# Kernel tuning notes

Measured on AMD Instinct MI355X. Metric: run time of the kernel, lower is better.

## Reference

```python
import jax, jax.numpy as jnp
import numpy as np

NUM_HEADS = 12
HEAD_DIM = 64
EPS = 1e-6


def _layernorm(x, g, b):
    mu = jnp.mean(x, axis=-1, keepdims=True)
    var = jnp.mean(jnp.square(x - mu), axis=-1, keepdims=True)
    return (x - mu) * jax.lax.rsqrt(var + EPS) * g + b


def setup_inputs() -> dict:
    key = jax.random.key(0)
    ks = jax.random.split(key, 8)
    D, DFF = 768, 3072
    s = lambda d: 1.0 / np.sqrt(d)
    return {
        "hidden_states": jax.random.normal(ks[0], (4, 2048, D), jnp.float32),
        "ln1_g": jnp.ones((D,), jnp.float32),
        "ln1_b": jnp.zeros((D,), jnp.float32),
        "w_qkv": jax.random.normal(ks[1], (D, 3 * D), jnp.float32) * s(D),
        "b_qkv": jnp.zeros((3 * D,), jnp.float32),
        "w_attn": jax.random.normal(ks[2], (D, D), jnp.float32) * s(D),
        "b_attn": jnp.zeros((D,), jnp.float32),
        "ln2_g": jnp.ones((D,), jnp.float32),
        "ln2_b": jnp.zeros((D,), jnp.float32),
        "w_in": jax.random.normal(ks[3], (D, DFF), jnp.float32) * s(D),
        "b_in": jnp.zeros((DFF,), jnp.float32),
        "w_out": jax.random.normal(ks[4], (DFF, D), jnp.float32) * s(DFF),
        "b_out": jnp.zeros((D,), jnp.float32),
    }


def reference(hidden_states, ln1_g, ln1_b, w_qkv, b_qkv, w_attn, b_attn,
              ln2_g, ln2_b, w_in, b_in, w_out, b_out):
    B, S, D = hidden_states.shape
    residual = hidden_states
    h = _layernorm(hidden_states, ln1_g, ln1_b)
    # QKV: [B,S,3D] -> [B,S,3,H,hd] -> [3,B,H,S,hd]
    qkv = (h @ w_qkv + b_qkv).reshape(B, S, 3, NUM_HEADS, HEAD_DIM)
    qkv = jnp.transpose(qkv, (2, 0, 3, 1, 4))
    scale = HEAD_DIM ** (-0.5)
    q, k, v = qkv[0] * scale, qkv[1], qkv[2]
    scores = jnp.einsum("bhqd,bhkd->bhqk", q, k)
    attn = jax.nn.softmax(scores, axis=-1)
    o = jnp.einsum("bhqk,bhkd->bhqd", attn, v)
    o = jnp.transpose(o, (0, 2, 1, 3)).reshape(B, S, D)
    h = residual + (o @ w_attn + b_attn)
    residual2 = h
    h2 = _layernorm(h, ln2_g, ln2_b)
    h2 = jax.nn.gelu(h2 @ w_in + b_in, approximate=False)
    h2 = h2 @ w_out + b_out
    return residual2 + h2
```

## Files before the change

### kernel.cpp

```cpp
#include <hip/hip_runtime.h>

typedef __bf16 bf16_t;
typedef bf16_t bf16x8 __attribute__((ext_vector_type(8)));
typedef float f32x4 __attribute__((ext_vector_type(4)));
typedef unsigned short ushortx8 __attribute__((ext_vector_type(8)));
typedef unsigned short ushortx4 __attribute__((ext_vector_type(4)));
typedef short short4v __attribute__((ext_vector_type(4)));

union UB8 { bf16_t h8[8]; bf16x8 b; };

__device__ __forceinline__ unsigned short f2bf(float f) {
  union { bf16_t h; unsigned short u; } cv;
  cv.h = (bf16_t)f;
  return cv.u;
}

__device__ __forceinline__ void gl_lds16(const unsigned short* g, unsigned short* l) {
  __builtin_amdgcn_global_load_lds((const __attribute__((address_space(1))) void*)g,
                                   (__attribute__((address_space(3))) void*)l,
                                   16, 0, 0);
}

__device__ __forceinline__ float gelu_fast(float v) {
  float v3 = v * v * v;
  float z = -2.30211886f * v - 0.102945f * v3;
  float e = exp2f(z);
  return v * __builtin_amdgcn_rcpf(1.0f + e);
}

__global__ __launch_bounds__(256) void ln_kernel(const float* __restrict__ x,
                                                 const float* __restrict__ g,
                                                 const float* __restrict__ b,
                                                 unsigned short* __restrict__ out) {
  int row = blockIdx.x;
  int t = threadIdx.x;
  const float* xr = x + (size_t)row * 768;
  float v0 = xr[t], v1 = xr[t + 256], v2 = xr[t + 512];
  __shared__ float red[4];
  float s = v0 + v1 + v2;
  for (int o = 32; o > 0; o >>= 1) s += __shfl_down(s, o, 64);
  if ((t & 63) == 0) red[t >> 6] = s;
  __syncthreads();
  float mu = (red[0] + red[1] + red[2] + red[3]) * (1.0f / 768.0f);
  __syncthreads();
  float d0 = v0 - mu, d1 = v1 - mu, d2 = v2 - mu;
  s = d0 * d0 + d1 * d1 + d2 * d2;
  for (int o = 32; o > 0; o >>= 1) s += __shfl_down(s, o, 64);
  if ((t & 63) == 0) red[t >> 6] = s;
  __syncthreads();
  float var = (red[0] + red[1] + red[2] + red[3]) * (1.0f / 768.0f);
  float rs = rsqrtf(var + 1e-6f);
  unsigned short* orow = out + (size_t)row * 768;
  orow[t]       = f2bf(d0 * rs * g[t]       + b[t]);
  orow[t + 256] = f2bf(d1 * rs * g[t + 256] + b[t + 256]);
  orow[t + 512] = f2bf(d2 * rs * g[t + 512] + b[t + 512]);
}

__global__ __launch_bounds__(256) void transpose_all(
    const float* __restrict__ w_qkv, const float* __restrict__ w_attn,
    const float* __restrict__ w_in, const float* __restrict__ w_out,
    unsigned short* __restrict__ wqkvT, unsigned short* __restrict__ wattnT,
    unsigned short* __restrict__ winT, unsigned short* __restrict__ woutT) {
  int id = blockIdx.x;
  const float* W; unsigned short* WT; int K, N, nx, ny;
  if (id < 1728)      { W = w_qkv;  WT = wqkvT;  K = 768;  N = 2304; nx = id % 72; ny = id / 72; }
  else if (id < 2304) { id -= 1728; W = w_attn; WT = wattnT; K = 768;  N = 768;  nx = id % 24; ny = id / 24; }
  else if (id < 4608) { id -= 2304; W = w_in;   WT = winT;   K = 768;  N = 3072; nx = id % 96; ny = id / 96; }
  else                { id -= 4608; W = w_out;  WT = woutT;  K = 3072; N = 768;  nx = id % 24; ny = id / 24; }
  __shared__ float tile[32][33];
  int n0 = nx * 32, k0 = ny * 32;
  int tx = threadIdx.x, ty = threadIdx.y;
  for (int i = 0; i < 4; i++)
    tile[ty + i * 8][tx] = W[(size_t)(k0 + ty + i * 8) * N + n0 + tx];
  __syncthreads();
  for (int i = 0; i < 4; i++)
    WT[(size_t)(n0 + ty + i * 8) * K + k0 + tx] = f2bf(tile[tx][ty + i * 8]);
}

template <int EPI>
__device__ __forceinline__ void gemm_body(const unsigned short* __restrict__ A,
                                          const unsigned short* __restrict__ BT,
                                          const float* __restrict__ bias,
                                          const float* resid,
                                          void* out, unsigned short* vt, int os,
                                          int N, int K) {
  constexpr int TM = 128, BK = 32, MI = 4;
  constexpr int ASZ = TM * BK;
  constexpr int BUF = ASZ + 128 * BK;
  __shared__ __align__(16) unsigned short smem[3 * BUF];

  int t = threadIdx.x;
  int w = t >> 6, lane = t & 63, ln = lane & 15, quad = lane >> 4;
  int wm = w & 1, wn = w >> 1;

  int gx = gridDim.x;
  int nwg = gx * gridDim.y;
  int flat = blockIdx.y * gx + blockIdx.x;
  int nf = (flat & 7) * (nwg >> 3) + (flat >> 3);
  int m0 = (nf / gx) * TM, n0 = (nf % gx) * 128;

  int lrow = lane >> 2;
  int lslot = lane & 3;
  int scol = (lslot ^ ((lrow >> 1) & 3)) * 8;

  const unsigned short* gA0 = A + (size_t)(m0 + w * 16 + lrow) * K + scol;
  const unsigned short* gA1 = gA0 + (size_t)64 * K;
  const unsigned short* gB0 = BT + (size_t)(n0 + w * 16 + lrow) * K + scol;
  const unsigned short* gB1 = gB0 + (size_t)64 * K;

  auto stage = [&](int buf) {
    unsigned short* Sb = smem + buf * BUF;
    gl_lds16(gA0, Sb + w * 512);
    gl_lds16(gA1, Sb + 2048 + w * 512);
    gl_lds16(gB0, Sb + ASZ + w * 512);
    gl_lds16(gB1, Sb + ASZ + 2048 + w * 512);
    gA0 += BK; gA1 += BK; gB0 += BK; gB1 += BK;
  };

  f32x4 acc[MI][4];
  f32x4 zero = {0.f, 0.f, 0.f, 0.f};
  for (int mi = 0; mi < MI; mi++)
    for (int ni = 0; ni < 4; ni++) acc[mi][ni] = zero;

  int nk = K / BK;
  stage(0);
  stage(1);
  int cur = 0;
  int soff = (quad ^ ((ln >> 1) & 3)) * 8;
  for (int kt = 0; kt < nk; kt++) {
    if (kt < nk - 1) { asm volatile("s_waitcnt vmcnt(4)" ::: "memory"); }
    else             { asm volatile("s_waitcnt vmcnt(0)" ::: "memory"); }
    __builtin_amdgcn_s_barrier();
    __builtin_amdgcn_sched_barrier(0);
    int pre = cur + 2; if (pre >= 3) pre -= 3;
    if (kt + 2 < nk) stage(pre);
    const unsigned short* Sc = smem + cur * BUF;
    bf16x8 af[MI], bfr[4];
#pragma unroll
    for (int mi = 0; mi < MI; mi++)
      af[mi] = *(const bf16x8*)&Sc[(wm * 64 + mi * 16 + ln) * 32 + soff];
#pragma unroll
    for (int ni = 0; ni < 4; ni++)
      bfr[ni] = *(const bf16x8*)&Sc[ASZ + (wn * 64 + ni * 16 + ln) * 32 + soff];
#pragma unroll
    for (int mi = 0; mi < MI; mi++)
#pragma unroll
      for (int ni = 0; ni < 4; ni++)
        acc[mi][ni] = __builtin_amdgcn_mfma_f32_16x16x32_bf16(af[mi], bfr[ni],
                                                              acc[mi][ni], 0, 0, 0);
    cur = cur + 1; if (cur >= 3) cur = 0;
  }

  if (EPI == 2) {
    float* outp = (float*)out;
    for (int mi = 0; mi < MI; mi++) {
      for (int ni = 0; ni < 4; ni++) {
        int col = n0 + wn * 64 + ni * 16 + ln;
        float bv = bias[col];
        for (int r = 0; r < 4; r++) {
          int row = m0 + wm * 64 + mi * 16 + quad * 4 + r;
          float v = acc[mi][ni][r] + bv;
          v += resid[(size_t)row * N + col];
          outp[(size_t)row * N + col] = v;
        }
      }
    }
  } else {
    __syncthreads();
    unsigned short* Cs16 = smem + w * 1024;
    unsigned short* outp = (unsigned short*)out;
    for (int mi = 0; mi < MI; mi++) {
      for (int ni = 0; ni < 4; ni++) {
        int col = n0 + wn * 64 + ni * 16 + ln;
        float bv = bias[col];
        for (int r = 0; r < 4; r++) {
          float v = acc[mi][ni][r] + bv;
          if (EPI == 0) {
            if (col < 768) v *= 0.18033688f;
          } else {
            v = gelu_fast(v);
          }
          Cs16[(quad * 4 + r) * 64 + ni * 16 + ln] = f2bf(v);
        }
      }
      __syncthreads();
      if (EPI == 0 && n0 >= 1536) {
        int c = n0 - 1536 + wn * 64 + lane;
        int s0 = m0 + wm * 64 + mi * 16;
        int bb = s0 >> 11, sl = s0 & 2047;
        ushortx8 lo, hi;
        for (int r = 0; r < 8; r++) lo[r] = Cs16[r * 64 + lane];
        for (int r = 0; r < 8; r++) hi[r] = Cs16[(8 + r) * 64 + lane];
        size_t vbase = ((size_t)(bb * 768 + c)) * 2048 + sl;
        *(ushortx8*)&vt[vbase] = lo;
        *(ushortx8*)&vt[vbase + 8] = hi;
      } else {
        int OS = (EPI == 0) ? os : N;
        for (int j = 0; j < 2; j++) {
          int rrow = j * 8 + (lane >> 3);
          int ch = (lane & 7) * 8;
          ushortx8 pv = *(const ushortx8*)&Cs16[rrow * 64 + ch];
          *(ushortx8*)&outp[(size_t)(m0 + wm * 64 + mi * 16 + rrow) * OS +
                            n0 + wn * 64 + ch] = pv;
        }
      }
      __syncthreads();
    }
  }
}

__global__ __launch_bounds__(256) void gemm_qkv(const unsigned short* A,
    const unsigned short* BT, const float* bias, void* out, unsigned short* vt,
    int N, int K) {
  gemm_body<0>(A, BT, bias, nullptr, out, vt, 1536, N, K);
}
__global__ __launch_bounds__(256) void gemm_attnout(const unsigned short* A,
    const unsigned short* BT, const float* bias, const float* resid, void* out,
    int N, int K) {
  gemm_body<2>(A, BT, bias, resid, out, nullptr, N, N, K);
}
__global__ __launch_bounds__(256) void gemm_ffn1(const unsigned short* A,
    const unsigned short* BT, const float* bias, void* out, int N, int K) {
  gemm_body<1>(A, BT, bias, nullptr, out, nullptr, N, N, K);
}
__global__ __launch_bounds__(256) void gemm_ffn2(const unsigned short* A,
    const unsigned short* BT, const float* bias, const float* resid, void* out,
    int N, int K) {
  gemm_body<2>(A, BT, bias, resid, out, nullptr, N, N, K);
}

__global__ __launch_bounds__(512, 4) void flash_attn(
    const unsigned short* __restrict__ qk, const unsigned short* __restrict__ v_t,
    unsigned short* __restrict__ o) {
  int flat = blockIdx.y * 16 + blockIdx.x;
  int nf = (flat & 7) * 96 + (flat >> 3);
  int qt = nf % 16;
  int bh = nf / 16;
  int b = bh / 12, h = bh % 12;
  int t = threadIdx.x;
  int w = t >> 6, lane = t & 63, ln = lane & 15, quad = lane >> 4;
  int qg = w & 3, kh2 = w >> 2;

  __shared__ __align__(16) unsigned short smem[18432];
  int qrow0 = b * 2048 + qt * 128;
  int qw = qrow0 + qg * 32;

  bf16x8 qf[2][2];
  for (int qi = 0; qi < 2; qi++)
    for (int kh = 0; kh < 2; kh++)
      qf[qi][kh] = *(const bf16x8*)&qk[(size_t)(qw + qi * 16 + ln) * 1536 +
                                      h * 64 + kh * 32 + quad * 8];

  UB8 ones8;
#pragma unroll
  for (int r = 0; r < 8; r++) ones8.h8[r] = (bf16_t)1.0f;

  f32x4 zero = {0.f, 0.f, 0.f, 0.f};
  f32x4 o_acc[4][2];
  for (int df = 0; df < 4; df++)
    for (int qi = 0; qi < 2; qi++) o_acc[df][qi] = zero;
  f32x4 l_acc[2] = {zero, zero};

  int sr = t >> 3, sc = (t & 7) * 8;
  int ssr = (sr & 32) | (((sr >> 2) & 1) << 4) | (((sr >> 3) & 3) << 2) | (sr & 3);
  ushortx8 kreg = *(const ushortx8*)&qk[(size_t)(b * 2048 + sr) * 1536 + 768 + h * 64 + sc];
  ushortx8 vreg = *(const ushortx8*)&v_t[(size_t)(bh * 64 + sr) * 2048 + sc];

  for (int kt = 0; kt < 32; kt++) {
    unsigned short* Ks = smem + (kt & 1) * 9216;
    unsigned short* Vt = Ks + 4608;
    *(ushortx8*)&Ks[ssr * 72 + sc] = kreg;
    *(ushortx8*)&Vt[sr * 72 + sc] = vreg;
    __syncthreads();
    if (kt < 31) {
      int krow0 = b * 2048 + (kt + 1) * 64;
      kreg = *(const ushortx8*)&qk[(size_t)(krow0 + sr) * 1536 + 768 + h * 64 + sc];
      vreg = *(const ushortx8*)&v_t[(size_t)(bh * 64 + sr) * 2048 + (kt + 1) * 64 + sc];
    }

    UB8 pb[2];
#pragma unroll
    for (int kf = 0; kf < 2; kf++) {
      int krow = kh2 * 32 + kf * 16;
      f32x4 ST[2] = {zero, zero};
      bf16x8 kA0 = *(const bf16x8*)&Ks[(krow + ln) * 72 + quad * 8];
      bf16x8 kA1 = *(const bf16x8*)&Ks[(krow + ln) * 72 + 32 + quad * 8];
      __builtin_amdgcn_s_setprio(1);
#pragma unroll
      for (int qi = 0; qi < 2; qi++) {
        ST[qi] = __builtin_amdgcn_mfma_f32_16x16x32_bf16(kA0, qf[qi][0], ST[qi], 0, 0, 0);
        ST[qi] = __builtin_amdgcn_mfma_f32_16x16x32_bf16(kA1, qf[qi][1], ST[qi], 0, 0, 0);
      }
      __builtin_amdgcn_s_setprio(0);
#pragma unroll
      for (int qi = 0; qi < 2; qi++)
#pragma unroll
        for (int r = 0; r < 4; r++)
          pb[qi].h8[kf * 4 + r] = (bf16_t)__builtin_amdgcn_exp2f(ST[qi][r]);
    }
    __builtin_amdgcn_s_setprio(1);
#pragma unroll
    for (int qi = 0; qi < 2; qi++)
      l_acc[qi] = __builtin_amdgcn_mfma_f32_16x16x32_bf16(ones8.b, pb[qi].b,
                                                          l_acc[qi], 0, 0, 0);
#pragma unroll
    for (int df = 0; df < 4; df++) {
      bf16x8 vA = *(const bf16x8*)&Vt[(df * 16 + ln) * 72 + kh2 * 32 + quad * 8];
#pragma unroll
      for (int qi = 0; qi < 2; qi++)
        o_acc[df][qi] = __builtin_amdgcn_mfma_f32_16x16x32_bf16(vA, pb[qi].b,
                                                                o_acc[df][qi], 0, 0, 0);
    }
    __builtin_amdgcn_s_setprio(0);
  }

  __syncthreads();
  float* fb = (float*)smem;
  float* fbl = fb + 8320;
  if (kh2 == 1) {
    for (int df = 0; df < 4; df++)
      for (int qi = 0; qi < 2; qi++)
        for (int r = 0; r < 4; r++)
          fb[qg * 2080 + (qi * 16 + ln) * 65 + df * 16 + quad * 4 + r] =
              o_acc[df][qi][r];
    if (quad == 0)
      for (int qi = 0; qi < 2; qi++)
        fbl[qg * 32 + qi * 16 + ln] = l_acc[qi][0];
  }
  __syncthreads();
  float inv[2];
  if (kh2 == 0) {
    for (int qi = 0; qi < 2; qi++) {
      float lt = l_acc[qi][0] + fbl[qg * 32 + qi * 16 + ln];
      inv[qi] = __builtin_amdgcn_rcpf(lt);
    }
    for (int df = 0; df < 4; df++)
      for (int qi = 0; qi < 2; qi++)
        for (int r = 0; r < 4; r++)
          o_acc[df][qi][r] += fb[qg * 2080 + (qi * 16 + ln) * 65 + df * 16 + quad * 4 + r];
  }
  __syncthreads();
  if (kh2 == 0) {
    unsigned short* Osm = smem + qg * 2304;
    for (int qi = 0; qi < 2; qi++)
      for (int df = 0; df < 4; df++)
        for (int r = 0; r < 4; r++)
          Osm[(qi * 16 + ln) * 72 + df * 16 + quad * 4 + r] =
              f2bf(o_acc[df][qi][r] * inv[qi]);
  }
  __syncthreads();
  if (kh2 == 0) {
    unsigned short* Osm = smem + qg * 2304;
    for (int p2 = 0; p2 < 4; p2++) {
      int rr = p2 * 8 + (lane >> 3);
      int ch = (lane & 7) * 8;
      ushortx8 u = *(const ushortx8*)&Osm[rr * 72 + ch];
      *(ushortx8*)&o[(size_t)(qw + rr) * 768 + h * 64 + ch] = u;
    }
  }
}

extern "C" void kernel_launch(void* const* d_in, const int* in_sizes, int n_in,
                              void* d_out, int out_size, void* d_ws, size_t ws_size,
                              hipStream_t stream) {
  const float* hidden = (const float*)d_in[0];
  const float* ln1_g  = (const float*)d_in[1];
  const float* ln1_b  = (const float*)d_in[2];
  const float* w_qkv  = (const float*)d_in[3];
  const float* b_qkv  = (const float*)d_in[4];
  const float* w_attn = (const float*)d_in[5];
  const float* b_attn = (const float*)d_in[6];
  const float* ln2_g  = (const float*)d_in[7];
  const float* ln2_b  = (const float*)d_in[8];
  const float* w_in   = (const float*)d_in[9];
  const float* b_in   = (const float*)d_in[10];
  const float* w_out  = (const float*)d_in[11];
  const float* b_out  = (const float*)d_in[12];
  float* out = (float*)d_out;

  char* ws = (char*)d_ws;
  unsigned short* wqkvT  = (unsigned short*)(ws + 0);
  unsigned short* wattnT = (unsigned short*)(ws + 3538944);
  unsigned short* winT   = (unsigned short*)(ws + 4718592);
  unsigned short* woutT  = (unsigned short*)(ws + 9437184);
  unsigned short* bufX   = (unsigned short*)(ws + 14155776);
  unsigned short* bufBig = (unsigned short*)(ws + 26738688);
  unsigned short* bufQK  = bufBig;
  unsigned short* v_t    = (unsigned short*)(ws + 26738688 + 25165824);

  transpose_all<<<6912, dim3(32, 8), 0, stream>>>(w_qkv, w_attn, w_in, w_out,
                                                  wqkvT, wattnT, winT, woutT);
  ln_kernel<<<8192, 256, 0, stream>>>(hidden, ln1_g, ln1_b, bufX);
  gemm_qkv<<<dim3(18, 64), 256, 0, stream>>>(bufX, wqkvT, b_qkv, (void*)bufQK,
                                             v_t, 2304, 768);
  flash_attn<<<dim3(16, 48), 512, 0, stream>>>(bufQK, v_t, bufX);
  gemm_attnout<<<dim3(6, 64), 256, 0, stream>>>(bufX, wattnT, b_attn, hidden,
                                                (void*)out, 768, 768);
  ln_kernel<<<8192, 256, 0, stream>>>(out, ln2_g, ln2_b, bufX);
  gemm_ffn1<<<dim3(24, 64), 256, 0, stream>>>(bufX, winT, b_in, (void*)bufBig,
                                              3072, 768);
  gemm_ffn2<<<dim3(6, 64), 256, 0, stream>>>(bufBig, woutT, b_out, out,
                                             (void*)out, 768, 3072);
}
```

Baseline: 382.3 us.

## Split-K FFN2 with atomic accumulation and use 64-row tiles for attn-out GEMM

The attention output projection now uses a 64-row M tile, doubling its grid to 768 blocks so more compute units are occupied. The FFN2 GEMM is split across two K chunks along grid z, and each chunk atomically adds its partial result into the output, which already holds the residual. Only the first chunk adds the bias. This raises parallelism for the skinny N=768 GEMMs, at the cost of fp32 atomic traffic and summation order that is no longer deterministic.

```diff
diff --git a/kernel.cpp b/kernel.cpp
--- a/kernel.cpp
+++ b/kernel.cpp
@@ -77,14 +77,14 @@
     WT[(size_t)(n0 + ty + i * 8) * K + k0 + tx] = f2bf(tile[tx][ty + i * 8]);
 }
 
-template <int EPI>
+template <int EPI, int TM>
 __device__ __forceinline__ void gemm_body(const unsigned short* __restrict__ A,
                                           const unsigned short* __restrict__ BT,
                                           const float* __restrict__ bias,
                                           const float* resid,
                                           void* out, unsigned short* vt, int os,
                                           int N, int K) {
-  constexpr int TM = 128, BK = 32, MI = 4;
+  constexpr int BK = 32, MI = TM / 32;
   constexpr int ASZ = TM * BK;
   constexpr int BUF = ASZ + 128 * BK;
   __shared__ __align__(16) unsigned short smem[3 * BUF];
@@ -99,22 +99,25 @@
   int nf = (flat & 7) * (nwg >> 3) + (flat >> 3);
   int m0 = (nf / gx) * TM, n0 = (nf % gx) * 128;
 
+  int Kc = (EPI == 3) ? (K / (int)gridDim.z) : K;
+  int kbase = (EPI == 3) ? ((int)blockIdx.z * Kc) : 0;
+
   int lrow = lane >> 2;
   int lslot = lane & 3;
   int scol = (lslot ^ ((lrow >> 1) & 3)) * 8;
 
-  const unsigned short* gA0 = A + (size_t)(m0 + w * 16 + lrow) * K + scol;
+  const unsigned short* gA0 = A + (size_t)(m0 + w * 16 + lrow) * K + kbase + scol;
   const unsigned short* gA1 = gA0 + (size_t)64 * K;
-  const unsigned short* gB0 = BT + (size_t)(n0 + w * 16 + lrow) * K + scol;
+  const unsigned short* gB0 = BT + (size_t)(n0 + w * 16 + lrow) * K + kbase + scol;
   const unsigned short* gB1 = gB0 + (size_t)64 * K;
 
   auto stage = [&](int buf) {
     unsigned short* Sb = smem + buf * BUF;
     gl_lds16(gA0, Sb + w * 512);
-    gl_lds16(gA1, Sb + 2048 + w * 512);
+    if constexpr (TM == 128) { gl_lds16(gA1, Sb + 2048 + w * 512); gA1 += BK; }
     gl_lds16(gB0, Sb + ASZ + w * 512);
     gl_lds16(gB1, Sb + ASZ + 2048 + w * 512);
-    gA0 += BK; gA1 += BK; gB0 += BK; gB1 += BK;
+    gA0 += BK; gB0 += BK; gB1 += BK;
   };
 
   f32x4 acc[MI][4];
@@ -122,14 +125,18 @@
   for (int mi = 0; mi < MI; mi++)
     for (int ni = 0; ni < 4; ni++) acc[mi][ni] = zero;
 
-  int nk = K / BK;
+  int nk = Kc / BK;
   stage(0);
   stage(1);
   int cur = 0;
   int soff = (quad ^ ((ln >> 1) & 3)) * 8;
   for (int kt = 0; kt < nk; kt++) {
-    if (kt < nk - 1) { asm volatile("s_waitcnt vmcnt(4)" ::: "memory"); }
-    else             { asm volatile("s_waitcnt vmcnt(0)" ::: "memory"); }
+    if (kt < nk - 1) {
+      if constexpr (TM == 128) asm volatile("s_waitcnt vmcnt(4)" ::: "memory");
+      else                     asm volatile("s_waitcnt vmcnt(3)" ::: "memory");
+    } else {
+      asm volatile("s_waitcnt vmcnt(0)" ::: "memory");
+    }
     __builtin_amdgcn_s_barrier();
     __builtin_amdgcn_sched_barrier(0);
     int pre = cur + 2; if (pre >= 3) pre -= 3;
@@ -138,7 +145,7 @@
     bf16x8 af[MI], bfr[4];
 #pragma unroll
     for (int mi = 0; mi < MI; mi++)
-      af[mi] = *(const bf16x8*)&Sc[(wm * 64 + mi * 16 + ln) * 32 + soff];
+      af[mi] = *(const bf16x8*)&Sc[(wm * (TM / 2) + mi * 16 + ln) * 32 + soff];
 #pragma unroll
     for (int ni = 0; ni < 4; ni++)
       bfr[ni] = *(const bf16x8*)&Sc[ASZ + (wn * 64 + ni * 16 + ln) * 32 + soff];
@@ -151,14 +158,27 @@
     cur = cur + 1; if (cur >= 3) cur = 0;
   }
 
-  if (EPI == 2) {
+  if (EPI == 3) {
+    float* outp = (float*)out;
+    bool addb = (blockIdx.z == 0);
+    for (int mi = 0; mi < MI; mi++) {
+      for (int ni = 0; ni < 4; ni++) {
+        int col = n0 + wn * 64 + ni * 16 + ln;
+        float bv = addb ? bias[col] : 0.0f;
+        for (int r = 0; r < 4; r++) {
+          int row = m0 + wm * (TM / 2) + mi * 16 + quad * 4 + r;
+          atomicAdd(&outp[(size_t)row * N + col], acc[mi][ni][r] + bv);
+        }
+      }
+    }
+  } else if (EPI == 2) {
     float* outp = (float*)out;
     for (int mi = 0; mi < MI; mi++) {
       for (int ni = 0; ni < 4; ni++) {
         int col = n0 + wn * 64 + ni * 16 + ln;
         float bv = bias[col];
         for (int r = 0; r < 4; r++) {
-          int row = m0 + wm * 64 + mi * 16 + quad * 4 + r;
+          int row = m0 + wm * (TM / 2) + mi * 16 + quad * 4 + r;
           float v = acc[mi][ni][r] + bv;
           v += resid[(size_t)row * N + col];
           outp[(size_t)row * N + col] = v;
@@ -186,7 +206,7 @@
       __syncthreads();
       if (EPI == 0 && n0 >= 1536) {
         int c = n0 - 1536 + wn * 64 + lane;
-        int s0 = m0 + wm * 64 + mi * 16;
+        int s0 = m0 + wm * (TM / 2) + mi * 16;
         int bb = s0 >> 11, sl = s0 & 2047;
         ushortx8 lo, hi;
         for (int r = 0; r < 8; r++) lo[r] = Cs16[r * 64 + lane];
@@ -200,7 +220,7 @@
           int rrow = j * 8 + (lane >> 3);
           int ch = (lane & 7) * 8;
           ushortx8 pv = *(const ushortx8*)&Cs16[rrow * 64 + ch];
-          *(ushortx8*)&outp[(size_t)(m0 + wm * 64 + mi * 16 + rrow) * OS +
+          *(ushortx8*)&outp[(size_t)(m0 + wm * (TM / 2) + mi * 16 + rrow) * OS +
                             n0 + wn * 64 + ch] = pv;
         }
       }
@@ -212,21 +232,21 @@
 __global__ __launch_bounds__(256) void gemm_qkv(const unsigned short* A,
     const unsigned short* BT, const float* bias, void* out, unsigned short* vt,
     int N, int K) {
-  gemm_body<0>(A, BT, bias, nullptr, out, vt, 1536, N, K);
+  gemm_body<0, 128>(A, BT, bias, nullptr, out, vt, 1536, N, K);
 }
 __global__ __launch_bounds__(256) void gemm_attnout(const unsigned short* A,
     const unsigned short* BT, const float* bias, const float* resid, void* out,
     int N, int K) {
-  gemm_body<2>(A, BT, bias, resid, out, nullptr, N, N, K);
+  gemm_body<2, 64>(A, BT, bias, resid, out, nullptr, N, N, K);
 }
 __global__ __launch_bounds__(256) void gemm_ffn1(const unsigned short* A,
     const unsigned short* BT, const float* bias, void* out, int N, int K) {
-  gemm_body<1>(A, BT, bias, nullptr, out, nullptr, N, N, K);
+  gemm_body<1, 128>(A, BT, bias, nullptr, out, nullptr, N, N, K);
 }
 __global__ __launch_bounds__(256) void gemm_ffn2(const unsigned short* A,
     const unsigned short* BT, const float* bias, const float* resid, void* out,
     int N, int K) {
-  gemm_body<2>(A, BT, bias, resid, out, nullptr, N, N, K);
+  gemm_body<3, 128>(A, BT, bias, resid, out, nullptr, N, N, K);
 }
 
 __global__ __launch_bounds__(512, 4) void flash_attn(
@@ -394,11 +414,11 @@
   gemm_qkv<<<dim3(18, 64), 256, 0, stream>>>(bufX, wqkvT, b_qkv, (void*)bufQK,
                                              v_t, 2304, 768);
   flash_attn<<<dim3(16, 48), 512, 0, stream>>>(bufQK, v_t, bufX);
-  gemm_attnout<<<dim3(6, 64), 256, 0, stream>>>(bufX, wattnT, b_attn, hidden,
-                                                (void*)out, 768, 768);
+  gemm_attnout<<<dim3(6, 128), 256, 0, stream>>>(bufX, wattnT, b_attn, hidden,
+                                                 (void*)out, 768, 768);
   ln_kernel<<<8192, 256, 0, stream>>>(out, ln2_g, ln2_b, bufX);
   gemm_ffn1<<<dim3(24, 64), 256, 0, stream>>>(bufX, winT, b_in, (void*)bufBig,
                                               3072, 768);
-  gemm_ffn2<<<dim3(6, 64), 256, 0, stream>>>(bufBig, woutT, b_out, out,
-                                             (void*)out, 768, 3072);
-}
+  gemm_ffn2<<<dim3(6, 64, 2), 256, 0, stream>>>(bufBig, woutT, b_out, nullptr,
+                                                (void*)out, 768, 3072);
+}
```

After: 373.3 us. -2.3%, faster.
